# Kernel optimization log

Measured on AMD Instinct MI355X. Metric: run time of the kernel, lower is better.

Reference implementation:

```python
import jax, jax.numpy as jnp
import numpy as np

B, T, D, H = 4096, 128, 32, 64

def _gru_layer(x, W_ih, W_hh, b_ih, b_hh):
    # x: [B, T, in]; W_ih: [3H, in]; W_hh: [3H, H]
    xg = jnp.einsum('bti,gi->btg', x, W_ih) + b_ih  # [B, T, 3H] input gates, one big GEMM
    def step(h, xg_t):
        gh = h @ W_hh.T + b_hh                      # [B, 3H]
        xr, xz, xn = jnp.split(xg_t, 3, axis=-1)
        hr, hz, hn = jnp.split(gh, 3, axis=-1)
        r = jax.nn.sigmoid(xr + hr)
        z = jax.nn.sigmoid(xz + hz)
        n = jnp.tanh(xn + r * hn)
        h_new = (1.0 - z) * n + z * h
        return h_new, h_new
    h0 = jnp.zeros((x.shape[0], W_hh.shape[1]), x.dtype)
    _, hs = jax.lax.scan(step, h0, jnp.swapaxes(xg, 0, 1))  # scan over time
    return jnp.swapaxes(hs, 0, 1)                   # [B, T, H]

def setup_inputs() -> dict:
    key = jax.random.key(0)
    ks = jax.random.split(key, 12)
    s = 0.1
    return {
        'x':     jax.random.normal(ks[0], (B, T, D), jnp.float32),
        'W_ih0': jax.random.normal(ks[1], (3 * H, D), jnp.float32) * s,
        'W_hh0': jax.random.normal(ks[2], (3 * H, H), jnp.float32) * s,
        'b_ih0': jax.random.normal(ks[3], (3 * H,), jnp.float32) * s,
        'b_hh0': jax.random.normal(ks[4], (3 * H,), jnp.float32) * s,
        'W_ih1': jax.random.normal(ks[5], (3 * H, H), jnp.float32) * s,
        'W_hh1': jax.random.normal(ks[6], (3 * H, H), jnp.float32) * s,
        'b_ih1': jax.random.normal(ks[7], (3 * H,), jnp.float32) * s,
        'b_hh1': jax.random.normal(ks[8], (3 * H,), jnp.float32) * s,
        'fc_w':  jax.random.normal(ks[9], (1, H), jnp.float32) * s,
        'fc_b':  jax.random.normal(ks[10], (1,), jnp.float32) * s,
    }

def reference(x, W_ih0, W_hh0, b_ih0, b_hh0, W_ih1, W_hh1, b_ih1, b_hh1, fc_w, fc_b):
    h1 = _gru_layer(x, W_ih0, W_hh0, b_ih0, b_hh0)   # layer 0
    h2 = _gru_layer(h1, W_ih1, W_hh1, b_ih1, b_hh1)  # layer 1
    last = h2[:, -1, :]                              # [B, H]
    out = last @ fc_w.T + fc_b                       # [B, 1]
    return jnp.squeeze(out, axis=-1)                 # [B]
```

## Files before the change

### kernel.cpp

```cpp
#include <hip/hip_runtime.h>

typedef _Float16 f16;
typedef f16 f16x8 __attribute__((ext_vector_type(8)));
typedef f16 f16x4 __attribute__((ext_vector_type(4)));
typedef __fp16 h16x2 __attribute__((ext_vector_type(2)));
typedef float f32x4 __attribute__((ext_vector_type(4)));
typedef float f32x2 __attribute__((ext_vector_type(2)));

#define MFMA16(A, B, C) __builtin_amdgcn_mfma_f32_16x16x32_f16((A), (B), (C), 0, 0, 0)

#define LDS_BARRIER() asm volatile("s_waitcnt lgkmcnt(0)\n\ts_barrier" ::: "memory")

__device__ __forceinline__ float E2(float x) {
#if __has_builtin(__builtin_amdgcn_exp2f)
  return __builtin_amdgcn_exp2f(x);
#else
  return __expf(x * 0.69314718056f);
#endif
}

__device__ __forceinline__ f16x8 cvt8(float4 a, float4 b) {
  union { h16x2 h[4]; f16x8 v; } u;
  u.h[0] = __builtin_amdgcn_cvt_pkrtz(a.x, a.y);
  u.h[1] = __builtin_amdgcn_cvt_pkrtz(a.z, a.w);
  u.h[2] = __builtin_amdgcn_cvt_pkrtz(b.x, b.y);
  u.h[3] = __builtin_amdgcn_cvt_pkrtz(b.z, b.w);
  return u.v;
}

__device__ __forceinline__ void gates_pair(f32x2 aR, f32x2 aZ, f32x2 aXN,
                                           f32x2 aHN, f32x2& hs) {
  const float K = -1.44269504f;
  f32x2 mR = aR * K;
  f32x2 mZ = aZ * K;
  f32x2 ea, eb;
  ea[0] = E2(mR[0]); ea[1] = E2(mR[1]);
  eb[0] = E2(mZ[0]); eb[1] = E2(mZ[1]);
  f32x2 pa = ea + 1.0f;
  f32x2 pb = eb + 1.0f;
  f32x2 prod = pa * pb;
  f32x2 inv;
  inv[0] = __builtin_amdgcn_rcpf(prod[0]);
  inv[1] = __builtin_amdgcn_rcpf(prod[1]);
  f32x2 rg = pb * inv;
  f32x2 zg = pa * inv;
  f32x2 y = rg * aHN + aXN;
  f32x2 my = y * (2.0f * K);
  f32x2 c;
  c[0] = E2(my[0]); c[1] = E2(my[1]);
  f32x2 num = 1.0f - c;
  f32x2 den = 1.0f + c;
  f32x2 rin;
  rin[0] = __builtin_amdgcn_rcpf(den[0]);
  rin[1] = __builtin_amdgcn_rcpf(den[1]);
  f32x2 ng = num * rin;
  hs = zg * (hs - ng) + ng;
}

__launch_bounds__(512, 2)
__global__ void gru_fused(const float* __restrict__ x,
                          const float* __restrict__ Wih0, const float* __restrict__ Whh0,
                          const float* __restrict__ bih0, const float* __restrict__ bhh0,
                          const float* __restrict__ Wih1, const float* __restrict__ Whh1,
                          const float* __restrict__ bih1, const float* __restrict__ bhh1,
                          const float* __restrict__ fcw, const float* __restrict__ fcb,
                          float* __restrict__ out) {
  __shared__ f16 H0[2][1024];
  __shared__ f16 H1[2][1024];
  __shared__ float red[4][16];

  const int tid = threadIdx.x;
  const int wave = tid >> 6;
  const int lane = tid & 63;
  const int l15 = lane & 15;
  const int q = lane >> 4;
  const int wa = wave & 3;
  const bool isB = wave >= 4;
  const int b0 = blockIdx.x * 16;

  for (int i = tid; i < 2048; i += 512) {
    ((f16*)H0)[i] = (f16)0.0f;
    ((f16*)H1)[i] = (f16)0.0f;
  }

  f16x8 wAx[3];
  f16x8 wAh[3][2];
  f16x8 wBx[3][2];
  f16x8 wBh[3][2];
  f32x4 bR, bZ, bXN, bHN;
  float fw[4] = {0.f, 0.f, 0.f, 0.f};

  if (!isB) {
#pragma unroll
    for (int g = 0; g < 3; ++g) {
      const int row = g * 64 + 16 * wa + l15;
      const float* p = Wih0 + row * 32 + q * 8;
      wAx[g] = cvt8(*(const float4*)p, *(const float4*)(p + 4));
#pragma unroll
      for (int kf = 0; kf < 2; ++kf) {
        const float* ph = Whh0 + row * 64 + kf * 32 + q * 8;
        wAh[g][kf] = cvt8(*(const float4*)ph, *(const float4*)(ph + 4));
      }
    }
#pragma unroll
    for (int r = 0; r < 4; ++r) {
      const int o = 16 * wa + 4 * q + r;
      bR[r] = bih0[o] + bhh0[o];
      bZ[r] = bih0[64 + o] + bhh0[64 + o];
      bXN[r] = bih0[128 + o];
      bHN[r] = bhh0[128 + o];
    }
  } else {
#pragma unroll
    for (int g = 0; g < 3; ++g) {
      const int row = g * 64 + 16 * wa + l15;
#pragma unroll
      for (int kf = 0; kf < 2; ++kf) {
        const float* p1 = Wih1 + row * 64 + kf * 32 + q * 8;
        wBx[g][kf] = cvt8(*(const float4*)p1, *(const float4*)(p1 + 4));
        const float* p2 = Whh1 + row * 64 + kf * 32 + q * 8;
        wBh[g][kf] = cvt8(*(const float4*)p2, *(const float4*)(p2 + 4));
      }
    }
#pragma unroll
    for (int r = 0; r < 4; ++r) {
      const int o = 16 * wa + 4 * q + r;
      bR[r] = bih1[o] + bhh1[o];
      bZ[r] = bih1[64 + o] + bhh1[64 + o];
      bXN[r] = bih1[128 + o];
      bHN[r] = bhh1[128 + o];
      fw[r] = fcw[o];
    }
  }
  const float fcb0 = fcb[0];

  f32x2 hs01 = {0.f, 0.f}, hs23 = {0.f, 0.f};

  const int wk0 = 16 * wa + 4 * q;
  const int widx = ((wk0 >> 3) * 16 + l15) * 8 + (wk0 & 7);

  auto stepA = [&](const f16* H0r, f16* H0w, float4 xav, float4 xbv) {
    const f16x8 xf = cvt8(xav, xbv);
    const f16x8 h0f0 = *(const f16x8*)&H0r[lane * 8];
    const f16x8 h0f1 = *(const f16x8*)&H0r[512 + lane * 8];
    f32x4 aR = bR, aZ = bZ, aXN = bXN, aHN = bHN;
    aR = MFMA16(wAx[0], xf, aR);
    aZ = MFMA16(wAx[1], xf, aZ);
    aXN = MFMA16(wAx[2], xf, aXN);
    aR = MFMA16(wAh[0][0], h0f0, aR);
    aZ = MFMA16(wAh[1][0], h0f0, aZ);
    aHN = MFMA16(wAh[2][0], h0f0, aHN);
    aR = MFMA16(wAh[0][1], h0f1, aR);
    aZ = MFMA16(wAh[1][1], h0f1, aZ);
    aHN = MFMA16(wAh[2][1], h0f1, aHN);
    gates_pair(f32x2{aR[0], aR[1]}, f32x2{aZ[0], aZ[1]},
               f32x2{aXN[0], aXN[1]}, f32x2{aHN[0], aHN[1]}, hs01);
    gates_pair(f32x2{aR[2], aR[3]}, f32x2{aZ[2], aZ[3]},
               f32x2{aXN[2], aXN[3]}, f32x2{aHN[2], aHN[3]}, hs23);
    union { h16x2 h2[2]; f16x4 v; } uw;
    uw.h2[0] = __builtin_amdgcn_cvt_pkrtz(hs01[0], hs01[1]);
    uw.h2[1] = __builtin_amdgcn_cvt_pkrtz(hs23[0], hs23[1]);
    *(f16x4*)&H0w[widx] = uw.v;
  };

  auto stepB = [&](const f16* H0r, const f16* H1r, f16* H1w) {
    const f16x8 g0 = *(const f16x8*)&H0r[lane * 8];
    const f16x8 g1 = *(const f16x8*)&H0r[512 + lane * 8];
    const f16x8 h1f0 = *(const f16x8*)&H1r[lane * 8];
    const f16x8 h1f1 = *(const f16x8*)&H1r[512 + lane * 8];
    f32x4 aR = bR, aZ = bZ, aXN = bXN, aHN = bHN;
    aR = MFMA16(wBx[0][0], g0, aR);
    aZ = MFMA16(wBx[1][0], g0, aZ);
    aXN = MFMA16(wBx[2][0], g0, aXN);
    aR = MFMA16(wBx[0][1], g1, aR);
    aZ = MFMA16(wBx[1][1], g1, aZ);
    aXN = MFMA16(wBx[2][1], g1, aXN);
    aR = MFMA16(wBh[0][0], h1f0, aR);
    aZ = MFMA16(wBh[1][0], h1f0, aZ);
    aHN = MFMA16(wBh[2][0], h1f0, aHN);
    aR = MFMA16(wBh[0][1], h1f1, aR);
    aZ = MFMA16(wBh[1][1], h1f1, aZ);
    aHN = MFMA16(wBh[2][1], h1f1, aHN);
    gates_pair(f32x2{aR[0], aR[1]}, f32x2{aZ[0], aZ[1]},
               f32x2{aXN[0], aXN[1]}, f32x2{aHN[0], aHN[1]}, hs01);
    gates_pair(f32x2{aR[2], aR[3]}, f32x2{aZ[2], aZ[3]},
               f32x2{aXN[2], aXN[3]}, f32x2{aHN[2], aHN[3]}, hs23);
    union { h16x2 h2[2]; f16x4 v; } uw;
    uw.h2[0] = __builtin_amdgcn_cvt_pkrtz(hs01[0], hs01[1]);
    uw.h2[1] = __builtin_amdgcn_cvt_pkrtz(hs23[0], hs23[1]);
    *(f16x4*)&H1w[widx] = uw.v;
  };

  __syncthreads();

  const float* xbase = x + (size_t)(b0 + l15) * 4096 + q * 8;
  float4 xa0, xb0, xa1, xb1;
  if (!isB) {
    xa0 = *(const float4*)xbase;
    xb0 = *(const float4*)(xbase + 4);
    xa1 = *(const float4*)(xbase + 32);
    xb1 = *(const float4*)(xbase + 36);
  }

  for (int t = 0; t < 128; t += 2) {
    if (!isB) {
      const float4 cxa = xa0, cxb = xb0;
      if (t + 2 < 128) {
        const float* xp = xbase + (t + 2) * 32;
        xa0 = *(const float4*)xp;
        xb0 = *(const float4*)(xp + 4);
      }
      stepA(H0[0], H0[1], cxa, cxb);
    } else if (t > 0) {
      stepB(H0[0], H1[0], H1[1]);
    }
    LDS_BARRIER();

    if (!isB) {
      const float4 cxa = xa1, cxb = xb1;
      if (t + 3 < 128) {
        const float* xp = xbase + (t + 3) * 32;
        xa1 = *(const float4*)xp;
        xb1 = *(const float4*)(xp + 4);
      }
      stepA(H0[1], H0[0], cxa, cxb);
    } else {
      stepB(H0[1], H1[1], H1[0]);
    }
    LDS_BARRIER();
  }
  if (isB) stepB(H0[0], H1[0], H1[1]);

  if (isB) {
    float partial = fw[0] * hs01[0] + fw[1] * hs01[1] + fw[2] * hs23[0] + fw[3] * hs23[1];
    partial += __shfl_down(partial, 16, 64);
    partial += __shfl_down(partial, 32, 64);
    if (lane < 16) red[wa][l15] = partial;
  }
  __syncthreads();
  if (tid < 16) out[b0 + tid] = red[0][tid] + red[1][tid] + red[2][tid] + red[3][tid] + fcb0;
}

extern "C" void kernel_launch(void* const* d_in, const int* in_sizes, int n_in,
                              void* d_out, int out_size, void* d_ws, size_t ws_size,
                              hipStream_t stream) {
  (void)in_sizes; (void)n_in; (void)out_size; (void)d_ws; (void)ws_size;
  const float* x    = (const float*)d_in[0];
  const float* Wih0 = (const float*)d_in[1];
  const float* Whh0 = (const float*)d_in[2];
  const float* bih0 = (const float*)d_in[3];
  const float* bhh0 = (const float*)d_in[4];
  const float* Wih1 = (const float*)d_in[5];
  const float* Whh1 = (const float*)d_in[6];
  const float* bih1 = (const float*)d_in[7];
  const float* bhh1 = (const float*)d_in[8];
  const float* fcw  = (const float*)d_in[9];
  const float* fcb  = (const float*)d_in[10];
  float* out = (float*)d_out;

  gru_fused<<<256, 512, 0, stream>>>(x, Wih0, Whh0, bih0, bhh0,
                                     Wih1, Whh1, bih1, bhh1, fcw, fcb, out);
}
```

Baseline: 176.7 us.

## Merge layer waves into one wave set and fold sigmoid/tanh scales into weights

Each of 4 waves now computes both GRU layers, where before 8 waves were split into a layer-0 group and a layer-1 group. The shared H0 fragment is read from LDS once and reused by both steps. The -log2(e) sigmoid and tanh scale factors are pre-multiplied into the fp16 weights and biases, which removes per-step scaling multiplies. This halves thread-level parallelism per block and serializes the two layers within each wave. Folding the scales into the fp16 weights may also slightly change rounding.

```diff
diff --git a/kernel.cpp b/kernel.cpp
--- a/kernel.cpp
+++ b/kernel.cpp
@@ -28,14 +28,29 @@
   return u.v;
 }
 
+__device__ __forceinline__ f16x8 cvt8s(const float* p, float s) {
+  float4 a = *(const float4*)p;
+  float4 b = *(const float4*)(p + 4);
+  union { h16x2 h[4]; f16x8 v; } u;
+  u.h[0] = __builtin_amdgcn_cvt_pkrtz(a.x * s, a.y * s);
+  u.h[1] = __builtin_amdgcn_cvt_pkrtz(a.z * s, a.w * s);
+  u.h[2] = __builtin_amdgcn_cvt_pkrtz(b.x * s, b.y * s);
+  u.h[3] = __builtin_amdgcn_cvt_pkrtz(b.z * s, b.w * s);
+  return u.v;
+}
+
+__device__ __forceinline__ f16x4 pack4(f32x2 a, f32x2 b) {
+  union { h16x2 h2[2]; f16x4 v; } u;
+  u.h2[0] = __builtin_amdgcn_cvt_pkrtz(a[0], a[1]);
+  u.h2[1] = __builtin_amdgcn_cvt_pkrtz(b[0], b[1]);
+  return u.v;
+}
+
 __device__ __forceinline__ void gates_pair(f32x2 aR, f32x2 aZ, f32x2 aXN,
                                            f32x2 aHN, f32x2& hs) {
-  const float K = -1.44269504f;
-  f32x2 mR = aR * K;
-  f32x2 mZ = aZ * K;
   f32x2 ea, eb;
-  ea[0] = E2(mR[0]); ea[1] = E2(mR[1]);
-  eb[0] = E2(mZ[0]); eb[1] = E2(mZ[1]);
+  ea[0] = E2(aR[0]); ea[1] = E2(aR[1]);
+  eb[0] = E2(aZ[0]); eb[1] = E2(aZ[1]);
   f32x2 pa = ea + 1.0f;
   f32x2 pb = eb + 1.0f;
   f32x2 prod = pa * pb;
@@ -44,8 +59,7 @@
   inv[1] = __builtin_amdgcn_rcpf(prod[1]);
   f32x2 rg = pb * inv;
   f32x2 zg = pa * inv;
-  f32x2 y = rg * aHN + aXN;
-  f32x2 my = y * (2.0f * K);
+  f32x2 my = aXN + rg * aHN;
   f32x2 c;
   c[0] = E2(my[0]); c[1] = E2(my[1]);
   f32x2 num = 1.0f - c;
@@ -57,7 +71,7 @@
   hs = zg * (hs - ng) + ng;
 }
 
-__launch_bounds__(512, 2)
+__launch_bounds__(256, 1)
 __global__ void gru_fused(const float* __restrict__ x,
                           const float* __restrict__ Wih0, const float* __restrict__ Whh0,
                           const float* __restrict__ bih0, const float* __restrict__ bhh0,
@@ -74,169 +88,144 @@
   const int lane = tid & 63;
   const int l15 = lane & 15;
   const int q = lane >> 4;
-  const int wa = wave & 3;
-  const bool isB = wave >= 4;
   const int b0 = blockIdx.x * 16;
 
-  for (int i = tid; i < 2048; i += 512) {
+  for (int i = tid; i < 2048; i += 256) {
     ((f16*)H0)[i] = (f16)0.0f;
     ((f16*)H1)[i] = (f16)0.0f;
   }
+
+  const float SRZ = -1.44269504f;
+  const float SN  = -2.88539008f;
 
   f16x8 wAx[3];
   f16x8 wAh[3][2];
   f16x8 wBx[3][2];
   f16x8 wBh[3][2];
-  f32x4 bR, bZ, bXN, bHN;
-  float fw[4] = {0.f, 0.f, 0.f, 0.f};
-
-  if (!isB) {
+  f32x4 bRA, bZA, bXNA, bHNA;
+  f32x4 bRB, bZB, bXNB, bHNB;
+  float fw[4];
+
 #pragma unroll
-    for (int g = 0; g < 3; ++g) {
-      const int row = g * 64 + 16 * wa + l15;
-      const float* p = Wih0 + row * 32 + q * 8;
-      wAx[g] = cvt8(*(const float4*)p, *(const float4*)(p + 4));
+  for (int g = 0; g < 3; ++g) {
+    const float s = (g == 2) ? SN : SRZ;
+    const int row = g * 64 + 16 * wave + l15;
+    wAx[g] = cvt8s(Wih0 + row * 32 + q * 8, s);
 #pragma unroll
-      for (int kf = 0; kf < 2; ++kf) {
-        const float* ph = Whh0 + row * 64 + kf * 32 + q * 8;
-        wAh[g][kf] = cvt8(*(const float4*)ph, *(const float4*)(ph + 4));
-      }
+    for (int kf = 0; kf < 2; ++kf) {
+      wAh[g][kf] = cvt8s(Whh0 + row * 64 + kf * 32 + q * 8, s);
+      wBx[g][kf] = cvt8s(Wih1 + row * 64 + kf * 32 + q * 8, s);
+      wBh[g][kf] = cvt8s(Whh1 + row * 64 + kf * 32 + q * 8, s);
     }
+  }
 #pragma unroll
-    for (int r = 0; r < 4; ++r) {
-      const int o = 16 * wa + 4 * q + r;
-      bR[r] = bih0[o] + bhh0[o];
-      bZ[r] = bih0[64 + o] + bhh0[64 + o];
-      bXN[r] = bih0[128 + o];
-      bHN[r] = bhh0[128 + o];
-    }
-  } else {
-#pragma unroll
-    for (int g = 0; g < 3; ++g) {
-      const int row = g * 64 + 16 * wa + l15;
-#pragma unroll
-      for (int kf = 0; kf < 2; ++kf) {
-        const float* p1 = Wih1 + row * 64 + kf * 32 + q * 8;
-        wBx[g][kf] = cvt8(*(const float4*)p1, *(const float4*)(p1 + 4));
-        const float* p2 = Whh1 + row * 64 + kf * 32 + q * 8;
-        wBh[g][kf] = cvt8(*(const float4*)p2, *(const float4*)(p2 + 4));
-      }
-    }
-#pragma unroll
-    for (int r = 0; r < 4; ++r) {
-      const int o = 16 * wa + 4 * q + r;
-      bR[r] = bih1[o] + bhh1[o];
-      bZ[r] = bih1[64 + o] + bhh1[64 + o];
-      bXN[r] = bih1[128 + o];
-      bHN[r] = bhh1[128 + o];
-      fw[r] = fcw[o];
-    }
+  for (int r = 0; r < 4; ++r) {
+    const int o = 16 * wave + 4 * q + r;
+    bRA[r]  = SRZ * (bih0[o] + bhh0[o]);
+    bZA[r]  = SRZ * (bih0[64 + o] + bhh0[64 + o]);
+    bXNA[r] = SN * bih0[128 + o];
+    bHNA[r] = SN * bhh0[128 + o];
+    bRB[r]  = SRZ * (bih1[o] + bhh1[o]);
+    bZB[r]  = SRZ * (bih1[64 + o] + bhh1[64 + o]);
+    bXNB[r] = SN * bih1[128 + o];
+    bHNB[r] = SN * bhh1[128 + o];
+    fw[r] = fcw[o];
   }
   const float fcb0 = fcb[0];
 
-  f32x2 hs01 = {0.f, 0.f}, hs23 = {0.f, 0.f};
-
-  const int wk0 = 16 * wa + 4 * q;
+  f32x2 hA01 = {0.f, 0.f}, hA23 = {0.f, 0.f};
+  f32x2 hB01 = {0.f, 0.f}, hB23 = {0.f, 0.f};
+
+  const int wk0 = 16 * wave + 4 * q;
   const int widx = ((wk0 >> 3) * 16 + l15) * 8 + (wk0 & 7);
 
-  auto stepA = [&](const f16* H0r, f16* H0w, float4 xav, float4 xbv) {
+  auto stepA = [&](f16x8 g0, f16x8 g1, f16* H0w, float4 xav, float4 xbv) {
     const f16x8 xf = cvt8(xav, xbv);
-    const f16x8 h0f0 = *(const f16x8*)&H0r[lane * 8];
-    const f16x8 h0f1 = *(const f16x8*)&H0r[512 + lane * 8];
-    f32x4 aR = bR, aZ = bZ, aXN = bXN, aHN = bHN;
-    aR = MFMA16(wAx[0], xf, aR);
-    aZ = MFMA16(wAx[1], xf, aZ);
-    aXN = MFMA16(wAx[2], xf, aXN);
-    aR = MFMA16(wAh[0][0], h0f0, aR);
-    aZ = MFMA16(wAh[1][0], h0f0, aZ);
-    aHN = MFMA16(wAh[2][0], h0f0, aHN);
-    aR = MFMA16(wAh[0][1], h0f1, aR);
-    aZ = MFMA16(wAh[1][1], h0f1, aZ);
-    aHN = MFMA16(wAh[2][1], h0f1, aHN);
+    f32x4 aR  = MFMA16(wAx[0], xf, bRA);
+    f32x4 aZ  = MFMA16(wAx[1], xf, bZA);
+    f32x4 aXN = MFMA16(wAx[2], xf, bXNA);
+    f32x4 aHN = MFMA16(wAh[2][0], g0, bHNA);
+    aR  = MFMA16(wAh[0][0], g0, aR);
+    aZ  = MFMA16(wAh[1][0], g0, aZ);
+    aR  = MFMA16(wAh[0][1], g1, aR);
+    aZ  = MFMA16(wAh[1][1], g1, aZ);
+    aHN = MFMA16(wAh[2][1], g1, aHN);
     gates_pair(f32x2{aR[0], aR[1]}, f32x2{aZ[0], aZ[1]},
-               f32x2{aXN[0], aXN[1]}, f32x2{aHN[0], aHN[1]}, hs01);
+               f32x2{aXN[0], aXN[1]}, f32x2{aHN[0], aHN[1]}, hA01);
     gates_pair(f32x2{aR[2], aR[3]}, f32x2{aZ[2], aZ[3]},
-               f32x2{aXN[2], aXN[3]}, f32x2{aHN[2], aHN[3]}, hs23);
-    union { h16x2 h2[2]; f16x4 v; } uw;
-    uw.h2[0] = __builtin_amdgcn_cvt_pkrtz(hs01[0], hs01[1]);
-    uw.h2[1] = __builtin_amdgcn_cvt_pkrtz(hs23[0], hs23[1]);
-    *(f16x4*)&H0w[widx] = uw.v;
+               f32x2{aXN[2], aXN[3]}, f32x2{aHN[2], aHN[3]}, hA23);
+    *(f16x4*)&H0w[widx] = pack4(hA01, hA23);
   };
 
-  auto stepB = [&](const f16* H0r, const f16* H1r, f16* H1w) {
-    const f16x8 g0 = *(const f16x8*)&H0r[lane * 8];
-    const f16x8 g1 = *(const f16x8*)&H0r[512 + lane * 8];
+  auto stepB = [&](f16x8 g0, f16x8 g1, const f16* H1r, f16* H1w) {
     const f16x8 h1f0 = *(const f16x8*)&H1r[lane * 8];
     const f16x8 h1f1 = *(const f16x8*)&H1r[512 + lane * 8];
-    f32x4 aR = bR, aZ = bZ, aXN = bXN, aHN = bHN;
-    aR = MFMA16(wBx[0][0], g0, aR);
-    aZ = MFMA16(wBx[1][0], g0, aZ);
-    aXN = MFMA16(wBx[2][0], g0, aXN);
-    aR = MFMA16(wBx[0][1], g1, aR);
-    aZ = MFMA16(wBx[1][1], g1, aZ);
+    f32x4 aR  = MFMA16(wBx[0][0], g0, bRB);
+    f32x4 aZ  = MFMA16(wBx[1][0], g0, bZB);
+    f32x4 aXN = MFMA16(wBx[2][0], g0, bXNB);
+    aR  = MFMA16(wBx[0][1], g1, aR);
+    aZ  = MFMA16(wBx[1][1], g1, aZ);
     aXN = MFMA16(wBx[2][1], g1, aXN);
-    aR = MFMA16(wBh[0][0], h1f0, aR);
-    aZ = MFMA16(wBh[1][0], h1f0, aZ);
-    aHN = MFMA16(wBh[2][0], h1f0, aHN);
-    aR = MFMA16(wBh[0][1], h1f1, aR);
-    aZ = MFMA16(wBh[1][1], h1f1, aZ);
+    f32x4 aHN = MFMA16(wBh[2][0], h1f0, bHNB);
+    aR  = MFMA16(wBh[0][0], h1f0, aR);
+    aZ  = MFMA16(wBh[1][0], h1f0, aZ);
+    aR  = MFMA16(wBh[0][1], h1f1, aR);
+    aZ  = MFMA16(wBh[1][1], h1f1, aZ);
     aHN = MFMA16(wBh[2][1], h1f1, aHN);
     gates_pair(f32x2{aR[0], aR[1]}, f32x2{aZ[0], aZ[1]},
-               f32x2{aXN[0], aXN[1]}, f32x2{aHN[0], aHN[1]}, hs01);
+               f32x2{aXN[0], aXN[1]}, f32x2{aHN[0], aHN[1]}, hB01);
     gates_pair(f32x2{aR[2], aR[3]}, f32x2{aZ[2], aZ[3]},
-               f32x2{aXN[2], aXN[3]}, f32x2{aHN[2], aHN[3]}, hs23);
-    union { h16x2 h2[2]; f16x4 v; } uw;
-    uw.h2[0] = __builtin_amdgcn_cvt_pkrtz(hs01[0], hs01[1]);
-    uw.h2[1] = __builtin_amdgcn_cvt_pkrtz(hs23[0], hs23[1]);
-    *(f16x4*)&H1w[widx] = uw.v;
+               f32x2{aXN[2], aXN[3]}, f32x2{aHN[2], aHN[3]}, hB23);
+    *(f16x4*)&H1w[widx] = pack4(hB01, hB23);
   };
 
   __syncthreads();
 
   const float* xbase = x + (size_t)(b0 + l15) * 4096 + q * 8;
-  float4 xa0, xb0, xa1, xb1;
-  if (!isB) {
-    xa0 = *(const float4*)xbase;
-    xb0 = *(const float4*)(xbase + 4);
-    xa1 = *(const float4*)(xbase + 32);
-    xb1 = *(const float4*)(xbase + 36);
-  }
+  float4 xa0 = *(const float4*)xbase;
+  float4 xb0 = *(const float4*)(xbase + 4);
+  float4 xa1 = *(const float4*)(xbase + 32);
+  float4 xb1 = *(const float4*)(xbase + 36);
 
   for (int t = 0; t < 128; t += 2) {
-    if (!isB) {
+    {
+      const f16x8 g0 = *(const f16x8*)&H0[0][lane * 8];
+      const f16x8 g1 = *(const f16x8*)&H0[0][512 + lane * 8];
       const float4 cxa = xa0, cxb = xb0;
       if (t + 2 < 128) {
         const float* xp = xbase + (t + 2) * 32;
         xa0 = *(const float4*)xp;
         xb0 = *(const float4*)(xp + 4);
       }
-      stepA(H0[0], H0[1], cxa, cxb);
-    } else if (t > 0) {
-      stepB(H0[0], H1[0], H1[1]);
+      if (t > 0) stepB(g0, g1, H1[0], H1[1]);
+      stepA(g0, g1, H0[1], cxa, cxb);
     }
     LDS_BARRIER();
 
-    if (!isB) {
+    {
+      const f16x8 g0 = *(const f16x8*)&H0[1][lane * 8];
+      const f16x8 g1 = *(const f16x8*)&H0[1][512 + lane * 8];
       const float4 cxa = xa1, cxb = xb1;
       if (t + 3 < 128) {
         const float* xp = xbase + (t + 3) * 32;
         xa1 = *(const float4*)xp;
         xb1 = *(const float4*)(xp + 4);
       }
-      stepA(H0[1], H0[0], cxa, cxb);
-    } else {
-      stepB(H0[1], H1[1], H1[0]);
+      stepB(g0, g1, H1[1], H1[0]);
+      stepA(g0, g1, H0[0], cxa, cxb);
     }
     LDS_BARRIER();
   }
-  if (isB) stepB(H0[0], H1[0], H1[1]);
-
-  if (isB) {
-    float partial = fw[0] * hs01[0] + fw[1] * hs01[1] + fw[2] * hs23[0] + fw[3] * hs23[1];
-    partial += __shfl_down(partial, 16, 64);
-    partial += __shfl_down(partial, 32, 64);
-    if (lane < 16) red[wa][l15] = partial;
-  }
+  {
+    const f16x8 g0 = *(const f16x8*)&H0[0][lane * 8];
+    const f16x8 g1 = *(const f16x8*)&H0[0][512 + lane * 8];
+    stepB(g0, g1, H1[0], H1[1]);
+  }
+
+  float partial = fw[0] * hB01[0] + fw[1] * hB01[1] + fw[2] * hB23[0] + fw[3] * hB23[1];
+  partial += __shfl_down(partial, 16, 64);
+  partial += __shfl_down(partial, 32, 64);
+  if (lane < 16) red[wave][l15] = partial;
   __syncthreads();
   if (tid < 16) out[b0 + tid] = red[0][tid] + red[1][tid] + red[2][tid] + red[3][tid] + fcb0;
 }
@@ -258,6 +247,6 @@
   const float* fcb  = (const float*)d_in[10];
   float* out = (float*)d_out;
 
-  gru_fused<<<256, 512, 0, stream>>>(x, Wih0, Whh0, bih0, bhh0,
+  gru_fused<<<256, 256, 0, stream>>>(x, Wih0, Whh0, bih0, bhh0,
                                      Wih1, Whh1, bih1, bhh1, fcw, fcb, out);
 }
```

New measurement: 200.3 us. 13.4% more time.

## Halve batch per block to double grid and fold gate scales into weights

Applied to the files above, without the earlier changes.

Each block now handles 8 batch rows instead of 16 and the grid doubles to 512 blocks, so more CUs are busy on the latency-bound recurrence. Half of each 16-wide MFMA tile is wasted on padding rows, which are clamped when loading x. The sigmoid and tanh exp2 scale constants are folded into the fp16 weights and biases, removing per-step multiplies. Launch bounds are raised to 4 blocks per CU, which may limit registers.

```diff
diff --git a/kernel.cpp b/kernel.cpp
--- a/kernel.cpp
+++ b/kernel.cpp
@@ -28,14 +28,29 @@
   return u.v;
 }
 
+__device__ __forceinline__ f16x8 cvt8s(const float* p, float s) {
+  float4 a = *(const float4*)p;
+  float4 b = *(const float4*)(p + 4);
+  union { h16x2 h[4]; f16x8 v; } u;
+  u.h[0] = __builtin_amdgcn_cvt_pkrtz(a.x * s, a.y * s);
+  u.h[1] = __builtin_amdgcn_cvt_pkrtz(a.z * s, a.w * s);
+  u.h[2] = __builtin_amdgcn_cvt_pkrtz(b.x * s, b.y * s);
+  u.h[3] = __builtin_amdgcn_cvt_pkrtz(b.z * s, b.w * s);
+  return u.v;
+}
+
+__device__ __forceinline__ f16x4 pack4(f32x2 a, f32x2 b) {
+  union { h16x2 h2[2]; f16x4 v; } u;
+  u.h2[0] = __builtin_amdgcn_cvt_pkrtz(a[0], a[1]);
+  u.h2[1] = __builtin_amdgcn_cvt_pkrtz(b[0], b[1]);
+  return u.v;
+}
+
 __device__ __forceinline__ void gates_pair(f32x2 aR, f32x2 aZ, f32x2 aXN,
                                            f32x2 aHN, f32x2& hs) {
-  const float K = -1.44269504f;
-  f32x2 mR = aR * K;
-  f32x2 mZ = aZ * K;
   f32x2 ea, eb;
-  ea[0] = E2(mR[0]); ea[1] = E2(mR[1]);
-  eb[0] = E2(mZ[0]); eb[1] = E2(mZ[1]);
+  ea[0] = E2(aR[0]); ea[1] = E2(aR[1]);
+  eb[0] = E2(aZ[0]); eb[1] = E2(aZ[1]);
   f32x2 pa = ea + 1.0f;
   f32x2 pb = eb + 1.0f;
   f32x2 prod = pa * pb;
@@ -44,8 +59,7 @@
   inv[1] = __builtin_amdgcn_rcpf(prod[1]);
   f32x2 rg = pb * inv;
   f32x2 zg = pa * inv;
-  f32x2 y = rg * aHN + aXN;
-  f32x2 my = y * (2.0f * K);
+  f32x2 my = aXN + rg * aHN;
   f32x2 c;
   c[0] = E2(my[0]); c[1] = E2(my[1]);
   f32x2 num = 1.0f - c;
@@ -57,7 +71,7 @@
   hs = zg * (hs - ng) + ng;
 }
 
-__launch_bounds__(512, 2)
+__launch_bounds__(512, 4)
 __global__ void gru_fused(const float* __restrict__ x,
                           const float* __restrict__ Wih0, const float* __restrict__ Whh0,
                           const float* __restrict__ bih0, const float* __restrict__ bhh0,
@@ -76,12 +90,15 @@
   const int q = lane >> 4;
   const int wa = wave & 3;
   const bool isB = wave >= 4;
-  const int b0 = blockIdx.x * 16;
+  const int b0 = blockIdx.x * 8;
 
   for (int i = tid; i < 2048; i += 512) {
     ((f16*)H0)[i] = (f16)0.0f;
     ((f16*)H1)[i] = (f16)0.0f;
   }
+
+  const float SRZ = -1.44269504f;
+  const float SN  = -2.88539008f;
 
   f16x8 wAx[3];
   f16x8 wAh[3][2];
@@ -93,42 +110,40 @@
   if (!isB) {
 #pragma unroll
     for (int g = 0; g < 3; ++g) {
+      const float s = (g == 2) ? SN : SRZ;
       const int row = g * 64 + 16 * wa + l15;
-      const float* p = Wih0 + row * 32 + q * 8;
-      wAx[g] = cvt8(*(const float4*)p, *(const float4*)(p + 4));
+      wAx[g] = cvt8s(Wih0 + row * 32 + q * 8, s);
 #pragma unroll
       for (int kf = 0; kf < 2; ++kf) {
-        const float* ph = Whh0 + row * 64 + kf * 32 + q * 8;
-        wAh[g][kf] = cvt8(*(const float4*)ph, *(const float4*)(ph + 4));
+        wAh[g][kf] = cvt8s(Whh0 + row * 64 + kf * 32 + q * 8, s);
       }
     }
 #pragma unroll
     for (int r = 0; r < 4; ++r) {
       const int o = 16 * wa + 4 * q + r;
-      bR[r] = bih0[o] + bhh0[o];
-      bZ[r] = bih0[64 + o] + bhh0[64 + o];
-      bXN[r] = bih0[128 + o];
-      bHN[r] = bhh0[128 + o];
+      bR[r]  = SRZ * (bih0[o] + bhh0[o]);
+      bZ[r]  = SRZ * (bih0[64 + o] + bhh0[64 + o]);
+      bXN[r] = SN * bih0[128 + o];
+      bHN[r] = SN * bhh0[128 + o];
     }
   } else {
 #pragma unroll
     for (int g = 0; g < 3; ++g) {
+      const float s = (g == 2) ? SN : SRZ;
       const int row = g * 64 + 16 * wa + l15;
 #pragma unroll
       for (int kf = 0; kf < 2; ++kf) {
-        const float* p1 = Wih1 + row * 64 + kf * 32 + q * 8;
-        wBx[g][kf] = cvt8(*(const float4*)p1, *(const float4*)(p1 + 4));
-        const float* p2 = Whh1 + row * 64 + kf * 32 + q * 8;
-        wBh[g][kf] = cvt8(*(const float4*)p2, *(const float4*)(p2 + 4));
+        wBx[g][kf] = cvt8s(Wih1 + row * 64 + kf * 32 + q * 8, s);
+        wBh[g][kf] = cvt8s(Whh1 + row * 64 + kf * 32 + q * 8, s);
       }
     }
 #pragma unroll
     for (int r = 0; r < 4; ++r) {
       const int o = 16 * wa + 4 * q + r;
-      bR[r] = bih1[o] + bhh1[o];
-      bZ[r] = bih1[64 + o] + bhh1[64 + o];
-      bXN[r] = bih1[128 + o];
-      bHN[r] = bhh1[128 + o];
+      bR[r]  = SRZ * (bih1[o] + bhh1[o]);
+      bZ[r]  = SRZ * (bih1[64 + o] + bhh1[64 + o]);
+      bXN[r] = SN * bih1[128 + o];
+      bHN[r] = SN * bhh1[128 + o];
       fw[r] = fcw[o];
     }
   }
@@ -143,24 +158,20 @@
     const f16x8 xf = cvt8(xav, xbv);
     const f16x8 h0f0 = *(const f16x8*)&H0r[lane * 8];
     const f16x8 h0f1 = *(const f16x8*)&H0r[512 + lane * 8];
-    f32x4 aR = bR, aZ = bZ, aXN = bXN, aHN = bHN;
-    aR = MFMA16(wAx[0], xf, aR);
-    aZ = MFMA16(wAx[1], xf, aZ);
-    aXN = MFMA16(wAx[2], xf, aXN);
-    aR = MFMA16(wAh[0][0], h0f0, aR);
-    aZ = MFMA16(wAh[1][0], h0f0, aZ);
-    aHN = MFMA16(wAh[2][0], h0f0, aHN);
-    aR = MFMA16(wAh[0][1], h0f1, aR);
-    aZ = MFMA16(wAh[1][1], h0f1, aZ);
+    f32x4 aR  = MFMA16(wAx[0], xf, bR);
+    f32x4 aZ  = MFMA16(wAx[1], xf, bZ);
+    f32x4 aXN = MFMA16(wAx[2], xf, bXN);
+    f32x4 aHN = MFMA16(wAh[2][0], h0f0, bHN);
+    aR  = MFMA16(wAh[0][0], h0f0, aR);
+    aZ  = MFMA16(wAh[1][0], h0f0, aZ);
+    aR  = MFMA16(wAh[0][1], h0f1, aR);
+    aZ  = MFMA16(wAh[1][1], h0f1, aZ);
     aHN = MFMA16(wAh[2][1], h0f1, aHN);
     gates_pair(f32x2{aR[0], aR[1]}, f32x2{aZ[0], aZ[1]},
                f32x2{aXN[0], aXN[1]}, f32x2{aHN[0], aHN[1]}, hs01);
     gates_pair(f32x2{aR[2], aR[3]}, f32x2{aZ[2], aZ[3]},
                f32x2{aXN[2], aXN[3]}, f32x2{aHN[2], aHN[3]}, hs23);
-    union { h16x2 h2[2]; f16x4 v; } uw;
-    uw.h2[0] = __builtin_amdgcn_cvt_pkrtz(hs01[0], hs01[1]);
-    uw.h2[1] = __builtin_amdgcn_cvt_pkrtz(hs23[0], hs23[1]);
-    *(f16x4*)&H0w[widx] = uw.v;
+    *(f16x4*)&H0w[widx] = pack4(hs01, hs23);
   };
 
   auto stepB = [&](const f16* H0r, const f16* H1r, f16* H1w) {
@@ -168,32 +179,29 @@
     const f16x8 g1 = *(const f16x8*)&H0r[512 + lane * 8];
     const f16x8 h1f0 = *(const f16x8*)&H1r[lane * 8];
     const f16x8 h1f1 = *(const f16x8*)&H1r[512 + lane * 8];
-    f32x4 aR = bR, aZ = bZ, aXN = bXN, aHN = bHN;
-    aR = MFMA16(wBx[0][0], g0, aR);
-    aZ = MFMA16(wBx[1][0], g0, aZ);
-    aXN = MFMA16(wBx[2][0], g0, aXN);
-    aR = MFMA16(wBx[0][1], g1, aR);
-    aZ = MFMA16(wBx[1][1], g1, aZ);
+    f32x4 aR  = MFMA16(wBx[0][0], g0, bR);
+    f32x4 aZ  = MFMA16(wBx[1][0], g0, bZ);
+    f32x4 aXN = MFMA16(wBx[2][0], g0, bXN);
+    aR  = MFMA16(wBx[0][1], g1, aR);
+    aZ  = MFMA16(wBx[1][1], g1, aZ);
     aXN = MFMA16(wBx[2][1], g1, aXN);
-    aR = MFMA16(wBh[0][0], h1f0, aR);
-    aZ = MFMA16(wBh[1][0], h1f0, aZ);
-    aHN = MFMA16(wBh[2][0], h1f0, aHN);
-    aR = MFMA16(wBh[0][1], h1f1, aR);
-    aZ = MFMA16(wBh[1][1], h1f1, aZ);
+    f32x4 aHN = MFMA16(wBh[2][0], h1f0, bHN);
+    aR  = MFMA16(wBh[0][0], h1f0, aR);
+    aZ  = MFMA16(wBh[1][0], h1f0, aZ);
+    aR  = MFMA16(wBh[0][1], h1f1, aR);
+    aZ  = MFMA16(wBh[1][1], h1f1, aZ);
     aHN = MFMA16(wBh[2][1], h1f1, aHN);
     gates_pair(f32x2{aR[0], aR[1]}, f32x2{aZ[0], aZ[1]},
                f32x2{aXN[0], aXN[1]}, f32x2{aHN[0], aHN[1]}, hs01);
     gates_pair(f32x2{aR[2], aR[3]}, f32x2{aZ[2], aZ[3]},
                f32x2{aXN[2], aXN[3]}, f32x2{aHN[2], aHN[3]}, hs23);
-    union { h16x2 h2[2]; f16x4 v; } uw;
-    uw.h2[0] = __builtin_amdgcn_cvt_pkrtz(hs01[0], hs01[1]);
-    uw.h2[1] = __builtin_amdgcn_cvt_pkrtz(hs23[0], hs23[1]);
-    *(f16x4*)&H1w[widx] = uw.v;
+    *(f16x4*)&H1w[widx] = pack4(hs01, hs23);
   };
 
   __syncthreads();
 
-  const float* xbase = x + (size_t)(b0 + l15) * 4096 + q * 8;
+  const int bb = min(b0 + l15, 4095);
+  const float* xbase = x + (size_t)bb * 4096 + q * 8;
   float4 xa0, xb0, xa1, xb1;
   if (!isB) {
     xa0 = *(const float4*)xbase;
@@ -238,7 +246,7 @@
     if (lane < 16) red[wa][l15] = partial;
   }
   __syncthreads();
-  if (tid < 16) out[b0 + tid] = red[0][tid] + red[1][tid] + red[2][tid] + red[3][tid] + fcb0;
+  if (tid < 8) out[b0 + tid] = red[0][tid] + red[1][tid] + red[2][tid] + red[3][tid] + fcb0;
 }
 
 extern "C" void kernel_launch(void* const* d_in, const int* in_sizes, int n_in,
@@ -258,6 +266,6 @@
   const float* fcb  = (const float*)d_in[10];
   float* out = (float*)d_out;
 
-  gru_fused<<<256, 512, 0, stream>>>(x, Wih0, Whh0, bih0, bhh0,
+  gru_fused<<<512, 512, 0, stream>>>(x, Wih0, Whh0, bih0, bhh0,
                                      Wih1, Whh1, bih1, bhh1, fcw, fcb, out);
 }
```

Measured after the change: 432.3 us. 145% more time.
